# Performance work log

Hardware: AMD Instinct MI355X
Metric: run time of the kernel (lower is better)

Reference implementation:

```python
import jax, jax.numpy as jnp
import numpy as np
from jax import lax

PATCH = 8  # patch_size = num_heads
DN = ('NCHW', 'OIHW', 'NCHW')


def setup_inputs() -> dict:
    key = jax.random.key(0)
    ks = jax.random.split(key, 4)
    b, c, H, W = 8, 64, 256, 256
    x = jax.random.normal(ks[0], (b, c, H, W), dtype=jnp.float32)
    qkv_w = jax.random.normal(ks[1], (3 * c, c, 1, 1), dtype=jnp.float32) * 0.05
    dw_w = jax.random.normal(ks[2], (3 * c, 1, 3, 3), dtype=jnp.float32) * 0.1
    proj_w = jax.random.normal(ks[3], (c, c, 1, 1), dtype=jnp.float32) * 0.05
    temperature = jnp.ones((c, 1, 1), dtype=jnp.float32)
    return {"x": x, "qkv_w": qkv_w, "dw_w": dw_w, "proj_w": proj_w,
            "temperature": temperature}


def _to_patches(t, p):
    b, c, H, W = t.shape
    # b c (h p1) (w p2) -> b c h w p1 p2
    t = t.reshape(b, c, H // p, p, W // p, p)
    return t.transpose(0, 1, 2, 4, 3, 5)


def _from_patches(t):
    b, c, h, w, p1, p2 = t.shape
    return t.transpose(0, 1, 2, 4, 3, 5).reshape(b, c, h * p1, w * p2)


def reference(x, qkv_w, dw_w, proj_w, temperature):
    p = PATCH
    c3 = qkv_w.shape[0]
    # 1x1 qkv projection then 3x3 depthwise conv (groups = 3*dim)
    qkv = lax.conv_general_dilated(x, qkv_w, (1, 1), 'SAME', dimension_numbers=DN)
    qkv = lax.conv_general_dilated(qkv, dw_w, (1, 1), 'SAME',
                                   dimension_numbers=DN, feature_group_count=c3)
    q, k, v = jnp.split(qkv, 3, axis=1)
    # FFT cross-correlation attention within p x p patches (fp32, matching .float())
    q_fft = jnp.fft.rfft2(_to_patches(q, p).astype(jnp.float32))
    k_fft = jnp.fft.rfft2(_to_patches(k, p).astype(jnp.float32))
    out = jnp.fft.irfft2(q_fft * k_fft, s=(p, p))
    out = _from_patches(out) * temperature  # temperature broadcasts [c,1,1]
    out = v * out
    out = lax.conv_general_dilated(out, proj_w, (1, 1), 'SAME', dimension_numbers=DN)
    return out
```

## Files before the change

### kernel.cpp

```cpp
#include <hip/hip_runtime.h>
#include <hip/hip_bf16.h>
#include <stdint.h>

#define BATCH 8
#define C 64
#define C3 192
#define HW 65536
#define NPIX (BATCH * HW)

typedef unsigned short u16;

typedef __bf16 bf16x8 __attribute__((ext_vector_type(8)));
typedef float f32x4 __attribute__((ext_vector_type(4)));

union FragU {
  bf16x8 v;
  u16 u[8];
  uint4 q;
};

__device__ __forceinline__ float bf2f(unsigned int u) {
  return __uint_as_float(u << 16);
}
__device__ __forceinline__ u16 f2bf(float f) {
  unsigned int x = __float_as_uint(f);
  unsigned int r = (x + 0x7fffu + ((x >> 16) & 1u)) >> 16;
  return (u16)r;
}

__device__ __forceinline__ void unpack8(uint4 v, float* f) {
  f[0] = bf2f(v.x & 0xffffu); f[1] = bf2f(v.x >> 16);
  f[2] = bf2f(v.y & 0xffffu); f[3] = bf2f(v.y >> 16);
  f[4] = bf2f(v.z & 0xffffu); f[5] = bf2f(v.z >> 16);
  f[6] = bf2f(v.w & 0xffffu); f[7] = bf2f(v.w >> 16);
}

__global__ void k0_det(const unsigned int* __restrict__ xbits,
                       int* __restrict__ flag) {
  __shared__ int cnt;
  if (threadIdx.x == 0) cnt = 0;
  __syncthreads();
  unsigned int u = xbits[threadIdx.x];
  int e = (u >> 7) & 0xff;
  int pred = (e >= 96 && e <= 134) ? 1 : 0;
  atomicAdd(&cnt, pred);
  __syncthreads();
  if (threadIdx.x == 0) *flag = (cnt >= 128) ? 1 : 0;
}

__global__ __launch_bounds__(256) void k1_mfma(const void* __restrict__ xv,
                                               const void* __restrict__ wv,
                                               u16* __restrict__ qkv1,
                                               const int* __restrict__ flag) {
  const int isbf = *flag;
  __shared__ u16 wl[C3 * C];
  for (int i = threadIdx.x; i < C3 * C; i += 256) {
    int row = i >> 6, col = i & 63;
    u16 b = isbf ? ((const u16*)wv)[i] : f2bf(((const float*)wv)[i]);
    int byt = row * 128 + ((col * 2) ^ ((row & 7) << 4));
    *(u16*)((char*)wl + byt) = b;
  }
  __syncthreads();

  const int w = threadIdx.x >> 6;
  const int l = threadIdx.x & 63;
  const int lg = l >> 4;
  const int lr = l & 15;
  const int n = blockIdx.x >> 8;
  const int hwbase = ((blockIdx.x & 255) << 8) + w * 64 + lr;

  FragU bfr[4][2];
  if (isbf) {
    const u16* xp = (const u16*)xv + (((size_t)n * C) << 16);
#pragma unroll
    for (int nt = 0; nt < 4; ++nt)
#pragma unroll
      for (int ks = 0; ks < 2; ++ks) {
        const u16* p = xp + (((size_t)(ks * 32 + lg * 8)) << 16) + hwbase + nt * 16;
#pragma unroll
        for (int e = 0; e < 8; ++e) bfr[nt][ks].u[e] = p[(size_t)e << 16];
      }
  } else {
    const float* xp = (const float*)xv + (((size_t)n * C) << 16);
#pragma unroll
    for (int nt = 0; nt < 4; ++nt)
#pragma unroll
      for (int ks = 0; ks < 2; ++ks) {
        const float* p = xp + (((size_t)(ks * 32 + lg * 8)) << 16) + hwbase + nt * 16;
#pragma unroll
        for (int e = 0; e < 8; ++e) bfr[nt][ks].u[e] = f2bf(p[(size_t)e << 16]);
      }
  }

#pragma unroll
  for (int mc = 0; mc < 4; ++mc) {
    bf16x8 af[3][2];
#pragma unroll
    for (int mt = 0; mt < 3; ++mt)
#pragma unroll
      for (int ks = 0; ks < 2; ++ks) {
        int row = mc * 48 + mt * 16 + lr;
        int colb = ks * 64 + lg * 16;
        FragU a;
        a.q = *(const uint4*)((const char*)wl + row * 128 +
                              (colb ^ ((row & 7) << 4)));
        af[mt][ks] = a.v;
      }
#pragma unroll
    for (int mt = 0; mt < 3; ++mt) {
#pragma unroll
      for (int nt = 0; nt < 4; ++nt) {
        f32x4 acc = {0.f, 0.f, 0.f, 0.f};
        acc = __builtin_amdgcn_mfma_f32_16x16x32_bf16(af[mt][0], bfr[nt][0].v,
                                                      acc, 0, 0, 0);
        acc = __builtin_amdgcn_mfma_f32_16x16x32_bf16(af[mt][1], bfr[nt][1].v,
                                                      acc, 0, 0, 0);
        int co = mc * 48 + mt * 16 + lg * 4;
        u16* op = qkv1 + (((size_t)(n * C3 + co)) << 16) + hwbase + nt * 16;
#pragma unroll
        for (int r = 0; r < 4; ++r) op[(size_t)r << 16] = f2bf(acc[r]);
      }
    }
  }
}

__global__ __launch_bounds__(256) void k2_dw(const u16* __restrict__ qkv1,
                                             const void* __restrict__ dwv,
                                             u16* __restrict__ qkv2,
                                             const int* __restrict__ flag) {
  const int isbf = *flag;
  unsigned int gg = blockIdx.x * 256 + threadIdx.x;
  int nc = (int)(gg >> 13);
  int rem = (int)(gg & 8191);
  int h = rem >> 5;
  int col0 = (rem & 31) * 8;
  int ch = nc % C3;

  float wv[9];
  if (isbf) {
    const u16* dw = (const u16*)dwv;
#pragma unroll
    for (int t = 0; t < 9; ++t) wv[t] = bf2f(dw[ch * 9 + t]);
  } else {
    const float* dw = (const float*)dwv;
#pragma unroll
    for (int t = 0; t < 9; ++t) wv[t] = dw[ch * 9 + t];
  }

  const u16* base = qkv1 + ((size_t)nc << 16);
  float acc[8];
#pragma unroll
  for (int j = 0; j < 8; ++j) acc[j] = 0.f;

#pragma unroll
  for (int kh = 0; kh < 3; ++kh) {
    int hh = h + kh - 1;
    if (hh < 0 || hh > 255) continue;
    const u16* rp = base + hh * 256 + col0;
    uint4 rv = *reinterpret_cast<const uint4*>(rp);
    float r[8];
    unpack8(rv, r);
    float lft = (col0 > 0) ? bf2f(rp[-1]) : 0.f;
    float rgt = (col0 < 248) ? bf2f(rp[8]) : 0.f;
    float w0 = wv[kh * 3], w1 = wv[kh * 3 + 1], w2 = wv[kh * 3 + 2];
    acc[0] += lft * w0 + r[0] * w1 + r[1] * w2;
#pragma unroll
    for (int j = 1; j < 7; ++j)
      acc[j] += r[j - 1] * w0 + r[j] * w1 + r[j + 1] * w2;
    acc[7] += r[6] * w0 + r[7] * w1 + rgt * w2;
  }

  unsigned int pk[4];
#pragma unroll
  for (int jj = 0; jj < 4; ++jj) {
    u16 lo = f2bf(acc[jj * 2]);
    u16 hi = f2bf(acc[jj * 2 + 1]);
    pk[jj] = (unsigned int)lo | ((unsigned int)hi << 16);
  }
  *reinterpret_cast<uint4*>(qkv2 + ((size_t)nc << 16) + h * 256 + col0) =
      make_uint4(pk[0], pk[1], pk[2], pk[3]);
}

__global__ __launch_bounds__(256) void k3_attn(const u16* __restrict__ qkv2,
                                               const void* __restrict__ tv,
                                               u16* __restrict__ voutb,
                                               const int* __restrict__ flag) {
  const int isbf = *flag;
  unsigned int g = blockIdx.x * 256 + threadIdx.x;
  int pw = g & 31;
  int ph = (g >> 5) & 31;
  int c = (g >> 10) & 63;
  int n = g >> 16;

  size_t pofs = (size_t)ph * (8 * 256) + (size_t)pw * 8;
  const u16* qp = qkv2 + (((size_t)(n * C3 + c)) << 16) + pofs;
  const u16* kp = qp + ((size_t)C << 16);
  const u16* vp = qp + ((size_t)(2 * C) << 16);

  float kreg[64];
#pragma unroll
  for (int r = 0; r < 8; ++r) {
    uint4 kv = *reinterpret_cast<const uint4*>(kp + r * 256);
    unpack8(kv, &kreg[r * 8]);
  }
  float acc[64];
#pragma unroll
  for (int i = 0; i < 64; ++i) acc[i] = 0.f;

#pragma unroll
  for (int a = 0; a < 8; ++a) {
    uint4 qv4 = *reinterpret_cast<const uint4*>(qp + a * 256);
    float qrow[8];
    unpack8(qv4, qrow);
#pragma unroll
    for (int b = 0; b < 8; ++b) {
      float qv = qrow[b];
#pragma unroll
      for (int i = 0; i < 8; ++i) {
#pragma unroll
        for (int j = 0; j < 8; ++j) {
          acc[i * 8 + j] += qv * kreg[((i - a) & 7) * 8 + ((j - b) & 7)];
        }
      }
    }
  }

  float tc = isbf ? bf2f(((const u16*)tv)[c]) : ((const float*)tv)[c];
  u16* op = voutb + (((size_t)(n * C + c)) << 16) + pofs;
#pragma unroll
  for (int i = 0; i < 8; ++i) {
    uint4 vv4 = *reinterpret_cast<const uint4*>(vp + i * 256);
    float vrow[8];
    unpack8(vv4, vrow);
    unsigned int pk[4];
#pragma unroll
    for (int jj = 0; jj < 4; ++jj) {
      u16 lo = f2bf(acc[i * 8 + jj * 2] * tc * vrow[jj * 2]);
      u16 hi = f2bf(acc[i * 8 + jj * 2 + 1] * tc * vrow[jj * 2 + 1]);
      pk[jj] = (unsigned int)lo | ((unsigned int)hi << 16);
    }
    *reinterpret_cast<uint4*>(op + i * 256) = make_uint4(pk[0], pk[1], pk[2], pk[3]);
  }
}

__global__ __launch_bounds__(256) void k4_mfma(const u16* __restrict__ vin,
                                               const void* __restrict__ pwv,
                                               float* __restrict__ outp,
                                               const int* __restrict__ flag) {
  const int isbf = *flag;
  __shared__ u16 wl[C * C];
  for (int i = threadIdx.x; i < C * C; i += 256) {
    int row = i >> 6, col = i & 63;
    u16 b = isbf ? ((const u16*)pwv)[i] : f2bf(((const float*)pwv)[i]);
    *(u16*)((char*)wl + row * 128 + ((col * 2) ^ ((row & 7) << 4))) = b;
  }
  __syncthreads();

  const int w = threadIdx.x >> 6;
  const int l = threadIdx.x & 63;
  const int lg = l >> 4, lr = l & 15;
  const int n = blockIdx.x >> 8;
  const int hwbase = ((blockIdx.x & 255) << 8) + w * 64 + lr;

  const u16* xp = vin + (((size_t)n * C) << 16);
  FragU bfr[4][2];
#pragma unroll
  for (int nt = 0; nt < 4; ++nt)
#pragma unroll
    for (int ks = 0; ks < 2; ++ks) {
      const u16* p = xp + (((size_t)(ks * 32 + lg * 8)) << 16) + hwbase + nt * 16;
#pragma unroll
      for (int e = 0; e < 8; ++e) bfr[nt][ks].u[e] = p[(size_t)e << 16];
    }

#pragma unroll
  for (int mt = 0; mt < 4; ++mt) {
    bf16x8 af[2];
#pragma unroll
    for (int ks = 0; ks < 2; ++ks) {
      int row = mt * 16 + lr;
      int colb = ks * 64 + lg * 16;
      FragU a;
      a.q = *(const uint4*)((const char*)wl + row * 128 +
                            (colb ^ ((row & 7) << 4)));
      af[ks] = a.v;
    }
#pragma unroll
    for (int nt = 0; nt < 4; ++nt) {
      f32x4 acc = {0.f, 0.f, 0.f, 0.f};
      acc = __builtin_amdgcn_mfma_f32_16x16x32_bf16(af[0], bfr[nt][0].v, acc, 0, 0, 0);
      acc = __builtin_amdgcn_mfma_f32_16x16x32_bf16(af[1], bfr[nt][1].v, acc, 0, 0, 0);
      int co = mt * 16 + lg * 4;
      float* op = outp + (((size_t)(n * C + co)) << 16) + hwbase + nt * 16;
#pragma unroll
      for (int r = 0; r < 4; ++r) op[(size_t)r << 16] = acc[r];
    }
  }
}

extern "C" void kernel_launch(void* const* d_in, const int* in_sizes, int n_in,
                              void* d_out, int out_size, void* d_ws, size_t ws_size,
                              hipStream_t stream) {
  const void* x = d_in[0];
  const void* qkv_w = d_in[1];
  const void* dw_w = d_in[2];
  const void* proj_w = d_in[3];
  const void* temp = d_in[4];

  u16* qkv1 = (u16*)d_ws;
  u16* qkv2 = qkv1 + (size_t)BATCH * C3 * HW;
  u16* voutb = (u16*)d_ws;
  int* flag = (int*)((char*)d_ws + (size_t)2 * BATCH * C3 * HW * 2);
  float* outp = (float*)d_out;

  k0_det<<<1, 256, 0, stream>>>((const unsigned int*)x, flag);
  k1_mfma<<<NPIX / 256, 256, 0, stream>>>(x, qkv_w, qkv1, flag);
  k2_dw<<<(BATCH * C3 * HW) / 8 / 256, 256, 0, stream>>>(qkv1, dw_w, qkv2, flag);
  k3_attn<<<NPIX / 256, 256, 0, stream>>>(qkv2, temp, voutb, flag);
  k4_mfma<<<NPIX / 256, 256, 0, stream>>>(voutb, proj_w, outp, flag);
}
```

Before: 596.4 us.

## Fuse depthwise conv and patch attention into one LDS-staged kernel

Merges the depthwise 3x3 conv and the circular-correlation attention into a single kernel. Each block stages an 8-row strip of q, k and v (with halo rows) in shared memory, runs the depthwise conv there, and then computes the patch correlation per output row. This removes the intermediate qkv2 write and read to global memory and one launch. It also spreads the per-patch work over 8 threads instead of one thread with 64-float accumulators, which lowers register pressure. The cost is extra shared-memory traffic and syncs, plus halo rows loaded redundantly.

After: 533.2 us. 10.6% less time.

```diff
diff --git a/kernel.cpp b/kernel.cpp
--- a/kernel.cpp
+++ b/kernel.cpp
@@ -124,123 +124,108 @@
   }
 }
 
-__global__ __launch_bounds__(256) void k2_dw(const u16* __restrict__ qkv1,
-                                             const void* __restrict__ dwv,
-                                             u16* __restrict__ qkv2,
-                                             const int* __restrict__ flag) {
+__global__ __launch_bounds__(256) void k23_fused(const u16* __restrict__ qkv1,
+                                                 const void* __restrict__ dwv,
+                                                 const void* __restrict__ tv,
+                                                 u16* __restrict__ voutb,
+                                                 const int* __restrict__ flag) {
   const int isbf = *flag;
-  unsigned int gg = blockIdx.x * 256 + threadIdx.x;
-  int nc = (int)(gg >> 13);
-  int rem = (int)(gg & 8191);
-  int h = rem >> 5;
-  int col0 = (rem & 31) * 8;
-  int ch = nc % C3;
-
-  float wv[9];
-  if (isbf) {
-    const u16* dw = (const u16*)dwv;
-#pragma unroll
-    for (int t = 0; t < 9; ++t) wv[t] = bf2f(dw[ch * 9 + t]);
-  } else {
-    const float* dw = (const float*)dwv;
-#pragma unroll
-    for (int t = 0; t < 9; ++t) wv[t] = dw[ch * 9 + t];
-  }
-
-  const u16* base = qkv1 + ((size_t)nc << 16);
-  float acc[8];
-#pragma unroll
-  for (int j = 0; j < 8; ++j) acc[j] = 0.f;
-
-#pragma unroll
-  for (int kh = 0; kh < 3; ++kh) {
-    int hh = h + kh - 1;
-    if (hh < 0 || hh > 255) continue;
-    const u16* rp = base + hh * 256 + col0;
-    uint4 rv = *reinterpret_cast<const uint4*>(rp);
-    float r[8];
-    unpack8(rv, r);
-    float lft = (col0 > 0) ? bf2f(rp[-1]) : 0.f;
-    float rgt = (col0 < 248) ? bf2f(rp[8]) : 0.f;
-    float w0 = wv[kh * 3], w1 = wv[kh * 3 + 1], w2 = wv[kh * 3 + 2];
-    acc[0] += lft * w0 + r[0] * w1 + r[1] * w2;
-#pragma unroll
-    for (int j = 1; j < 7; ++j)
-      acc[j] += r[j - 1] * w0 + r[j] * w1 + r[j + 1] * w2;
-    acc[7] += r[6] * w0 + r[7] * w1 + rgt * w2;
-  }
-
+  const int strip = blockIdx.x & 31;
+  const int c = (blockIdx.x >> 5) & 63;
+  const int n = blockIdx.x >> 11;
+  const int h0 = strip * 8;
+  const int tid = threadIdx.x;
+
+  __shared__ u16 in_s[3][10 * 256];
+  __shared__ float dw_s[3][32 * 65];
+
+  for (int idx = tid; idx < 3 * 10 * 32; idx += 256) {
+    int pl = idx / 320;
+    int rem = idx - pl * 320;
+    int r = rem >> 5;
+    int cg = rem & 31;
+    int gh = h0 + r - 1;
+    uint4 val = make_uint4(0u, 0u, 0u, 0u);
+    if (gh >= 0 && gh < 256) {
+      const u16* src = qkv1 + (((size_t)(n * C3 + c + 64 * pl)) << 16) +
+                       gh * 256 + cg * 8;
+      val = *reinterpret_cast<const uint4*>(src);
+    }
+    *reinterpret_cast<uint4*>(&in_s[pl][r * 256 + cg * 8]) = val;
+  }
+  __syncthreads();
+
+  const int row = tid >> 5;
+  const int pch = tid & 31;
+  const int col0 = pch * 8;
+
+  for (int pl = 0; pl < 3; ++pl) {
+    int ch = c + 64 * pl;
+    float wv9[9];
+    if (isbf) {
+      const u16* dw = (const u16*)dwv;
+#pragma unroll
+      for (int t = 0; t < 9; ++t) wv9[t] = bf2f(dw[ch * 9 + t]);
+    } else {
+      const float* dw = (const float*)dwv;
+#pragma unroll
+      for (int t = 0; t < 9; ++t) wv9[t] = dw[ch * 9 + t];
+    }
+    float acc[8];
+#pragma unroll
+    for (int j = 0; j < 8; ++j) acc[j] = 0.f;
+#pragma unroll
+    for (int kh = 0; kh < 3; ++kh) {
+      const u16* rp = &in_s[pl][(row + kh) * 256 + col0];
+      uint4 rv = *reinterpret_cast<const uint4*>(rp);
+      float r8[8];
+      unpack8(rv, r8);
+      float lft = (col0 > 0) ? bf2f(rp[-1]) : 0.f;
+      float rgt = (col0 < 248) ? bf2f(rp[8]) : 0.f;
+      float w0 = wv9[kh * 3], w1 = wv9[kh * 3 + 1], w2 = wv9[kh * 3 + 2];
+      acc[0] += lft * w0 + r8[0] * w1 + r8[1] * w2;
+#pragma unroll
+      for (int j = 1; j < 7; ++j)
+        acc[j] += r8[j - 1] * w0 + r8[j] * w1 + r8[j + 1] * w2;
+      acc[7] += r8[6] * w0 + r8[7] * w1 + rgt * w2;
+    }
+#pragma unroll
+    for (int j = 0; j < 8; ++j) dw_s[pl][pch * 65 + row * 8 + j] = acc[j];
+  }
+  __syncthreads();
+
+  const int s = row;
+  float acc8[8];
+#pragma unroll
+  for (int j = 0; j < 8; ++j) acc8[j] = 0.f;
+  const float* qb = &dw_s[0][pch * 65];
+  const float* kb = &dw_s[1][pch * 65];
+#pragma unroll
+  for (int a = 0; a < 8; ++a) {
+    int kr = (s - a) & 7;
+    float krow[8];
+#pragma unroll
+    for (int e = 0; e < 8; ++e) krow[e] = kb[kr * 8 + e];
+#pragma unroll
+    for (int b = 0; b < 8; ++b) {
+      float qab = qb[a * 8 + b];
+#pragma unroll
+      for (int j = 0; j < 8; ++j) acc8[j] += qab * krow[(j - b) & 7];
+    }
+  }
+
+  float tc = isbf ? bf2f(((const u16*)tv)[c]) : ((const float*)tv)[c];
+  const float* vb = &dw_s[2][pch * 65 + s * 8];
   unsigned int pk[4];
 #pragma unroll
   for (int jj = 0; jj < 4; ++jj) {
-    u16 lo = f2bf(acc[jj * 2]);
-    u16 hi = f2bf(acc[jj * 2 + 1]);
+    u16 lo = f2bf(acc8[jj * 2] * tc * vb[jj * 2]);
+    u16 hi = f2bf(acc8[jj * 2 + 1] * tc * vb[jj * 2 + 1]);
     pk[jj] = (unsigned int)lo | ((unsigned int)hi << 16);
   }
-  *reinterpret_cast<uint4*>(qkv2 + ((size_t)nc << 16) + h * 256 + col0) =
+  *reinterpret_cast<uint4*>(voutb + (((size_t)(n * C + c)) << 16) +
+                            (h0 + s) * 256 + pch * 8) =
       make_uint4(pk[0], pk[1], pk[2], pk[3]);
-}
-
-__global__ __launch_bounds__(256) void k3_attn(const u16* __restrict__ qkv2,
-                                               const void* __restrict__ tv,
-                                               u16* __restrict__ voutb,
-                                               const int* __restrict__ flag) {
-  const int isbf = *flag;
-  unsigned int g = blockIdx.x * 256 + threadIdx.x;
-  int pw = g & 31;
-  int ph = (g >> 5) & 31;
-  int c = (g >> 10) & 63;
-  int n = g >> 16;
-
-  size_t pofs = (size_t)ph * (8 * 256) + (size_t)pw * 8;
-  const u16* qp = qkv2 + (((size_t)(n * C3 + c)) << 16) + pofs;
-  const u16* kp = qp + ((size_t)C << 16);
-  const u16* vp = qp + ((size_t)(2 * C) << 16);
-
-  float kreg[64];
-#pragma unroll
-  for (int r = 0; r < 8; ++r) {
-    uint4 kv = *reinterpret_cast<const uint4*>(kp + r * 256);
-    unpack8(kv, &kreg[r * 8]);
-  }
-  float acc[64];
-#pragma unroll
-  for (int i = 0; i < 64; ++i) acc[i] = 0.f;
-
-#pragma unroll
-  for (int a = 0; a < 8; ++a) {
-    uint4 qv4 = *reinterpret_cast<const uint4*>(qp + a * 256);
-    float qrow[8];
-    unpack8(qv4, qrow);
-#pragma unroll
-    for (int b = 0; b < 8; ++b) {
-      float qv = qrow[b];
-#pragma unroll
-      for (int i = 0; i < 8; ++i) {
-#pragma unroll
-        for (int j = 0; j < 8; ++j) {
-          acc[i * 8 + j] += qv * kreg[((i - a) & 7) * 8 + ((j - b) & 7)];
-        }
-      }
-    }
-  }
-
-  float tc = isbf ? bf2f(((const u16*)tv)[c]) : ((const float*)tv)[c];
-  u16* op = voutb + (((size_t)(n * C + c)) << 16) + pofs;
-#pragma unroll
-  for (int i = 0; i < 8; ++i) {
-    uint4 vv4 = *reinterpret_cast<const uint4*>(vp + i * 256);
-    float vrow[8];
-    unpack8(vv4, vrow);
-    unsigned int pk[4];
-#pragma unroll
-    for (int jj = 0; jj < 4; ++jj) {
-      u16 lo = f2bf(acc[i * 8 + jj * 2] * tc * vrow[jj * 2]);
-      u16 hi = f2bf(acc[i * 8 + jj * 2 + 1] * tc * vrow[jj * 2 + 1]);
-      pk[jj] = (unsigned int)lo | ((unsigned int)hi << 16);
-    }
-    *reinterpret_cast<uint4*>(op + i * 256) = make_uint4(pk[0], pk[1], pk[2], pk[3]);
-  }
 }
 
 __global__ __launch_bounds__(256) void k4_mfma(const u16* __restrict__ vin,
@@ -308,14 +293,12 @@
   const void* temp = d_in[4];
 
   u16* qkv1 = (u16*)d_ws;
-  u16* qkv2 = qkv1 + (size_t)BATCH * C3 * HW;
-  u16* voutb = (u16*)d_ws;
+  u16* voutb = qkv1 + (size_t)BATCH * C3 * HW;
   int* flag = (int*)((char*)d_ws + (size_t)2 * BATCH * C3 * HW * 2);
   float* outp = (float*)d_out;
 
   k0_det<<<1, 256, 0, stream>>>((const unsigned int*)x, flag);
   k1_mfma<<<NPIX / 256, 256, 0, stream>>>(x, qkv_w, qkv1, flag);
-  k2_dw<<<(BATCH * C3 * HW) / 8 / 256, 256, 0, stream>>>(qkv1, dw_w, qkv2, flag);
-  k3_attn<<<NPIX / 256, 256, 0, stream>>>(qkv2, temp, voutb, flag);
+  k23_fused<<<BATCH * C * 32, 256, 0, stream>>>(qkv1, dw_w, temp, voutb, flag);
   k4_mfma<<<NPIX / 256, 256, 0, stream>>>(voutb, proj_w, outp, flag);
 }
```
